# Kernel tuning notes

Measured on AMD Instinct MI355X. Metric: run time of the kernel, lower is better.

Reference implementation:

```python
import jax, jax.numpy as jnp
import numpy as np

N, M = 20000, 5000
D_IN, D_OUT = 256, 512
EPS = 1e-5


def setup_inputs() -> dict:
    key = jax.random.key(0)
    k1, k2, k3, k4 = jax.random.split(key, 4)
    x = jax.random.normal(k1, (N, D_IN), dtype=jnp.float32)
    H = (jax.random.uniform(k2, (N, M)) < 0.05).astype(jnp.float32)
    W_node = jax.random.normal(k3, (D_IN, D_OUT), dtype=jnp.float32) / np.sqrt(D_IN)
    W_res = jax.random.normal(k4, (D_IN, D_OUT), dtype=jnp.float32) / np.sqrt(D_IN)
    gamma = jnp.ones((D_OUT,), dtype=jnp.float32)
    beta = jnp.zeros((D_OUT,), dtype=jnp.float32)
    return {"x": x, "H": H, "W_node": W_node, "W_res": W_res, "gamma": gamma, "beta": beta}


def reference(x, H, W_node, W_res, gamma, beta):
    # degrees, clamped to >= 1
    d_v = jnp.clip(jnp.sum(H, axis=1), 1.0)   # [N] node degree
    d_e = jnp.clip(jnp.sum(H, axis=0), 1.0)   # [M] hyperedge degree
    x_proj = x @ W_node                       # [N, d_out]
    edge_feat = (H.T @ x_proj) / d_e[:, None] # [M, d_out] node -> edge aggregation
    node_update = (H @ edge_feat) / d_v[:, None]  # [N, d_out] edge -> node
    h = node_update + x @ W_res               # residual (d_in != d_out -> linear)
    # LayerNorm over last dim
    mu = jnp.mean(h, axis=-1, keepdims=True)
    var = jnp.mean(jnp.square(h - mu), axis=-1, keepdims=True)
    out = (h - mu) * jax.lax.rsqrt(var + EPS) * gamma + beta
    return out  # dropout is identity at inference
```

## Files before the change

kernel.cpp:

```cpp
#include <hip/hip_runtime.h>


#define N_NODES 20000
#define M_EDGES 5000
#define MPAD    5120
#define NPAD    20480
#define NW      320
#define MW      80
#define DIN     256
#define DOUT    512
#define SPLITS  16
#define SPLITSB 4

typedef short bf16x4 __attribute__((ext_vector_type(4)));
typedef short bf16x8 __attribute__((ext_vector_type(8)));
typedef float f32x4 __attribute__((ext_vector_type(4)));
typedef unsigned long long u64;

#define MFMA16(A, B, C) __builtin_amdgcn_mfma_f32_16x16x32_bf16((A), (B), (C), 0, 0, 0)

__device__ __forceinline__ unsigned short f2b(float f) {
  unsigned u = __builtin_bit_cast(unsigned, f);
  return (unsigned short)((u + 0x7FFFu + ((u >> 16) & 1u)) >> 16);
}

__device__ __forceinline__ void stage16(const void* g, void* l) {
  __builtin_amdgcn_global_load_lds(
      (const __attribute__((address_space(1))) unsigned int*)g,
      (__attribute__((address_space(3))) unsigned int*)l, 16, 0, 0);
}

__device__ __forceinline__ bf16x8 expand8(unsigned b) {
  union { unsigned u[4]; bf16x8 v; } r;
  const unsigned t = b | (b << 15);
  r.u[0] = (t & 0x00010001u) * 0x3F80u;
  r.u[1] = ((t >> 2) & 0x00010001u) * 0x3F80u;
  r.u[2] = ((t >> 4) & 0x00010001u) * 0x3F80u;
  r.u[3] = ((t >> 6) & 0x00010001u) * 0x3F80u;
  return r.v;
}

__global__ __launch_bounds__(256) void prep_kernel(const float* __restrict__ Wn,
                                                   const float* __restrict__ Wr,
                                                   unsigned short* __restrict__ WT) {
  const int q = blockIdx.x * 256 + threadIdx.x;
  const int j = q >> 9, k = q & 511;
  const float v = (k < 256) ? Wn[(size_t)k * 512 + j] : Wr[(size_t)(k - 256) * 512 + j];
  WT[(size_t)j * 512 + k] = f2b(v);
}

__global__ __launch_bounds__(256) void xt_kernel(const float* __restrict__ x,
                                                 unsigned short* __restrict__ xpb) {
  const int j = threadIdx.x;
  const int n8 = blockIdx.x;
  union { unsigned u[4]; bf16x8 v; } o;
#pragma unroll
  for (int p = 0; p < 4; ++p) {
    const int n = n8 * 8 + 2 * p;
    const float v0 = (n < N_NODES) ? x[(size_t)n * DIN + j] : 0.f;
    const float v1 = (n + 1 < N_NODES) ? x[(size_t)(n + 1) * DIN + j] : 0.f;
    o.u[p] = (unsigned)f2b(v0) | ((unsigned)f2b(v1) << 16);
  }
  *(bf16x8*)(xpb + ((size_t)n8 * 256 + j) * 8) = o.v;
}

__global__ __launch_bounds__(256) void pack_kernel(const float* __restrict__ H,
                                                   u64* __restrict__ HTb) {
  const int t = threadIdx.x;
  const int g = blockIdx.x;
  const int h = blockIdx.y;
  const int n0 = g * 64;
  const int mc = h * 1024 + 4 * t;
  u64 h0 = 0, h1 = 0, h2 = 0, h3 = 0;
  if (mc + 3 < M_EDGES) {
    const float* col = H + mc;
#pragma unroll 4
    for (int r = 0; r < 64; ++r) {
      const int n = n0 + r;
      if (n < N_NODES) {
        const float4 v = *(const float4*)(col + (size_t)n * M_EDGES);
        h0 |= (u64)(v.x != 0.f) << r;
        h1 |= (u64)(v.y != 0.f) << r;
        h2 |= (u64)(v.z != 0.f) << r;
        h3 |= (u64)(v.w != 0.f) << r;
      }
    }
  } else if (mc < M_EDGES) {
    for (int r = 0; r < 64; ++r) {
      const int n = n0 + r;
      if (n < N_NODES) {
        const float* row = H + (size_t)n * M_EDGES;
        if (mc + 0 < M_EDGES) h0 |= (u64)(row[mc + 0] != 0.f) << r;
        if (mc + 1 < M_EDGES) h1 |= (u64)(row[mc + 1] != 0.f) << r;
        if (mc + 2 < M_EDGES) h2 |= (u64)(row[mc + 2] != 0.f) << r;
        if (mc + 3 < M_EDGES) h3 |= (u64)(row[mc + 3] != 0.f) << r;
      }
    }
  }
  u64* hp = HTb + (size_t)g * MPAD + mc;
  hp[0] = h0; hp[1] = h1; hp[2] = h2; hp[3] = h3;
}

__global__ __launch_bounds__(256) void bt_kernel(const u64* __restrict__ HTb,
                                                 u64* __restrict__ Hb) {
  const int t = threadIdx.x;
  const int w = t >> 6, l = t & 63;
  const int id = blockIdx.x * 4 + w;
  const int nw = id % NW;
  const int mw = id / NW;
  const u64 word = HTb[(size_t)nw * MPAD + mw * 64 + l];
  u64 out = 0;
  for (int r = 0; r < 64; ++r) {
    const u64 mask = __ballot(((word >> r) & 1ull) != 0);
    if (l == r) out = mask;
  }
  Hb[(size_t)mw * NPAD + nw * 64 + l] = out;
}

__global__ __launch_bounds__(256) void deg_kernel(const u64* __restrict__ Hb,
                                                  const u64* __restrict__ HTb,
                                                  float* __restrict__ inv_de,
                                                  float* __restrict__ inv_dv) {
  const int g = blockIdx.x * 256 + threadIdx.x;
  if (g < MPAD) {
    int c = 0;
    for (int nw = 0; nw < NW; ++nw) c += __popcll(HTb[(size_t)nw * MPAD + g]);
    inv_de[g] = 1.f / fmaxf((float)c, 1.f);
  } else if (g < MPAD + NPAD) {
    const int n = g - MPAD;
    int c = 0;
#pragma unroll
    for (int mw = 0; mw < MW; ++mw) c += __popcll(Hb[(size_t)mw * NPAD + n]);
    inv_dv[n] = 1.f / fmaxf((float)c, 1.f);
  }
}

__global__ __launch_bounds__(256) void gemmA_kernel(const unsigned short* __restrict__ xpb,
                                                    const u64* __restrict__ HTb,
                                                    float* __restrict__ partial) {
  __shared__ char lds[2][16384];
  const int t = threadIdx.x;
  const int w = t >> 6, l = t & 63;
  const int lr = l & 15, lg = l >> 4;
  const int shl8 = lg * 8;
  const int wgid = blockIdx.x;
  const int mchunk = wgid >> 6;
  const int sj = wgid & 63;
  const int s = sj >> 2, jb = sj & 3;
  const int m0 = mchunk * 256 + w * 64;
  const int j0 = jb * 64;

  f32x4 acc[4][4] = {};
  const u64* bbase = HTb + (size_t)(s * 20) * MPAD + m0 + lr;
  const char* xb = (const char*)xpb;
  const int n8b = s * 160;
  const int sj0 = j0 + w * 16 + lr;

  u64 b00, b01, b02, b03, b04, b05, b06, b07;
  u64 b10, b11, b12, b13, b14, b15, b16, b17;

#define GA_LOADB(S, st_) do {                                                  \
    const u64* bp_ = bbase + (size_t)(st_) * 2 * MPAD;                         \
    b##S##0 = bp_[0]; b##S##1 = bp_[16]; b##S##2 = bp_[32]; b##S##3 = bp_[48]; \
    const u64* bq_ = bp_ + MPAD;                                               \
    b##S##4 = bq_[0]; b##S##5 = bq_[16]; b##S##6 = bq_[32]; b##S##7 = bq_[48]; \
  } while (0)

#define GA_STAGE(buf, st_) do {                                                \
    const size_t r0_ = (size_t)(n8b + (st_) * 16 + lg) * 256 + sj0;            \
    stage16(xb + (r0_) * 16,              &lds[buf][(w) * 1024 + l * 16]);     \
    stage16(xb + (r0_ + 4 * 256) * 16,    &lds[buf][(4 + w) * 1024 + l * 16]); \
    stage16(xb + (r0_ + 8 * 256) * 16,    &lds[buf][(8 + w) * 1024 + l * 16]); \
    stage16(xb + (r0_ + 12 * 256) * 16,   &lds[buf][(12 + w) * 1024 + l * 16]);\
  } while (0)

#define GA_JG(jg, BW) do {                                                     \
    const unsigned wlo_ = (unsigned)(BW), whi_ = (unsigned)((BW) >> 32);       \
    const bf16x8 e0_ = expand8((wlo_ >> shl8) & 255u);                         \
    const bf16x8 e1_ = expand8((whi_ >> shl8) & 255u);                         \
    acc[0][jg] = MFMA16(A00_, e0_, acc[0][jg]);                                \
    acc[1][jg] = MFMA16(A10_, e0_, acc[1][jg]);                                \
    acc[2][jg] = MFMA16(A20_, e0_, acc[2][jg]);                                \
    acc[3][jg] = MFMA16(A30_, e0_, acc[3][jg]);                                \
    acc[0][jg] = MFMA16(A01_, e1_, acc[0][jg]);                                \
    acc[1][jg] = MFMA16(A11_, e1_, acc[1][jg]);                                \
    acc[2][jg] = MFMA16(A21_, e1_, acc[2][jg]);                                \
    acc[3][jg] = MFMA16(A31_, e1_, acc[3][jg]);                                \
  } while (0)

#define GA_COMP(buf, h, W0, W1, W2, W3) do {                                   \
    const char* L_ = &lds[buf][(h) * 8192];                                    \
    const bf16x8 A00_ = *(const bf16x8*)(L_ + l * 16 + 0);                     \
    const bf16x8 A10_ = *(const bf16x8*)(L_ + l * 16 + 1024);                  \
    const bf16x8 A20_ = *(const bf16x8*)(L_ + l * 16 + 2048);                  \
    const bf16x8 A30_ = *(const bf16x8*)(L_ + l * 16 + 3072);                  \
    const bf16x8 A01_ = *(const bf16x8*)(L_ + l * 16 + 4096);                  \
    const bf16x8 A11_ = *(const bf16x8*)(L_ + l * 16 + 5120);                  \
    const bf16x8 A21_ = *(const bf16x8*)(L_ + l * 16 + 6144);                  \
    const bf16x8 A31_ = *(const bf16x8*)(L_ + l * 16 + 7168);                  \
    GA_JG(0, W0); GA_JG(1, W1); GA_JG(2, W2); GA_JG(3, W3);                    \
  } while (0)

  GA_LOADB(0, 0);
  GA_STAGE(0, 0);
  for (int st = 0; st < 10; st += 2) {
    const int n1 = (st + 1 < 10) ? st + 1 : 9;
    GA_LOADB(1, n1); GA_STAGE(1, n1);
    asm volatile("s_waitcnt vmcnt(12)" ::: "memory");
    __builtin_amdgcn_s_barrier();
    GA_COMP(0, 0, b00, b01, b02, b03);
    GA_COMP(0, 1, b04, b05, b06, b07);
    __builtin_amdgcn_s_barrier();
    const int n2 = (st + 2 < 10) ? st + 2 : 9;
    GA_LOADB(0, n2); GA_STAGE(0, n2);
    asm volatile("s_waitcnt vmcnt(12)" ::: "memory");
    __builtin_amdgcn_s_barrier();
    GA_COMP(1, 0, b10, b11, b12, b13);
    GA_COMP(1, 1, b14, b15, b16, b17);
    __builtin_amdgcn_s_barrier();
  }
#undef GA_LOADB
#undef GA_STAGE
#undef GA_JG
#undef GA_COMP

  float* pp = partial + (size_t)s * (DIN * MPAD);
#pragma unroll
  for (int fr = 0; fr < 4; ++fr)
#pragma unroll
    for (int r = 0; r < 4; ++r) {
      const int j = j0 + fr * 16 + lg * 4 + r;
#pragma unroll
      for (int jg = 0; jg < 4; ++jg)
        pp[(size_t)j * MPAD + m0 + jg * 16 + lr] = acc[fr][jg][r];
    }
}

__global__ __launch_bounds__(256) void reduceA_kernel(const float* __restrict__ partial,
                                                      const float* __restrict__ inv_de,
                                                      unsigned short* __restrict__ t2p) {
  const int t = threadIdx.x;
  const int m = blockIdx.x * 256 + t;
  const int jc = blockIdx.y * 16;
  const float e = inv_de[m];
  unsigned short* ob = t2p + ((size_t)(m >> 3) * 256) * 8 + (m & 7);
  for (int jj = 0; jj < 16; ++jj) {
    const int j = jc + jj;
    const float* p = partial + (size_t)j * MPAD + m;
    float s = 0.f;
#pragma unroll
    for (int sp = 0; sp < SPLITS; ++sp) s += p[(size_t)sp * (DIN * MPAD)];
    ob[(size_t)j * 8] = f2b(s * e);
  }
}

__global__ __launch_bounds__(256) void gemmB_kernel(const unsigned short* __restrict__ t2p,
                                                    const u64* __restrict__ Hb,
                                                    float* __restrict__ partialB) {
  __shared__ char lds[2][16384];
  const int t = threadIdx.x;
  const int w = t >> 6, l = t & 63;
  const int lr = l & 15, lg = l >> 4;
  const int shl8 = lg * 8;
  const int wgid = blockIdx.x;
  const int nchunk = wgid >> 4;
  const int sj = wgid & 15;
  const int s = sj >> 2, jb = sj & 3;
  const int n0 = nchunk * 256 + w * 64;
  const int j0 = jb * 64;

  f32x4 acc[4][4] = {};
  const u64* abase = Hb + (size_t)(s * 20) * NPAD + n0 + lr;
  const char* tb = (const char*)t2p;
  const int m8b = s * 160;
  const int sj0 = j0 + w * 16 + lr;

  u64 a00, a01, a02, a03, a04, a05, a06, a07;
  u64 a10, a11, a12, a13, a14, a15, a16, a17;

#define GB_LOADA(S, st_) do {                                                  \
    const u64* ap_ = abase + (size_t)(st_) * 2 * NPAD;                         \
    a##S##0 = ap_[0]; a##S##1 = ap_[16]; a##S##2 = ap_[32]; a##S##3 = ap_[48]; \
    const u64* aq_ = ap_ + NPAD;                                               \
    a##S##4 = aq_[0]; a##S##5 = aq_[16]; a##S##6 = aq_[32]; a##S##7 = aq_[48]; \
  } while (0)

#define GB_STAGE(buf, st_) do {                                                \
    const size_t r0_ = (size_t)(m8b + (st_) * 16 + lg) * 256 + sj0;            \
    stage16(tb + (r0_) * 16,              &lds[buf][(w) * 1024 + l * 16]);     \
    stage16(tb + (r0_ + 4 * 256) * 16,    &lds[buf][(4 + w) * 1024 + l * 16]); \
    stage16(tb + (r0_ + 8 * 256) * 16,    &lds[buf][(8 + w) * 1024 + l * 16]); \
    stage16(tb + (r0_ + 12 * 256) * 16,   &lds[buf][(12 + w) * 1024 + l * 16]);\
  } while (0)

#define GB_FR(fr, AW) do {                                                     \
    const unsigned wlo_ = (unsigned)(AW), whi_ = (unsigned)((AW) >> 32);       \
    const bf16x8 e0_ = expand8((wlo_ >> shl8) & 255u);                         \
    const bf16x8 e1_ = expand8((whi_ >> shl8) & 255u);                         \
    acc[fr][0] = MFMA16(e0_, B00_, acc[fr][0]);                                \
    acc[fr][1] = MFMA16(e0_, B10_, acc[fr][1]);                                \
    acc[fr][2] = MFMA16(e0_, B20_, acc[fr][2]);                                \
    acc[fr][3] = MFMA16(e0_, B30_, acc[fr][3]);                                \
    acc[fr][0] = MFMA16(e1_, B01_, acc[fr][0]);                                \
    acc[fr][1] = MFMA16(e1_, B11_, acc[fr][1]);                                \
    acc[fr][2] = MFMA16(e1_, B21_, acc[fr][2]);                                \
    acc[fr][3] = MFMA16(e1_, B31_, acc[fr][3]);                                \
  } while (0)

#define GB_COMP(buf, h, W0, W1, W2, W3) do {                                   \
    const char* L_ = &lds[buf][(h) * 8192];                                    \
    const bf16x8 B00_ = *(const bf16x8*)(L_ + l * 16 + 0);                     \
    const bf16x8 B10_ = *(const bf16x8*)(L_ + l * 16 + 1024);                  \
    const bf16x8 B20_ = *(const bf16x8*)(L_ + l * 16 + 2048);                  \
    const bf16x8 B30_ = *(const bf16x8*)(L_ + l * 16 + 3072);                  \
    const bf16x8 B01_ = *(const bf16x8*)(L_ + l * 16 + 4096);                  \
    const bf16x8 B11_ = *(const bf16x8*)(L_ + l * 16 + 5120);                  \
    const bf16x8 B21_ = *(const bf16x8*)(L_ + l * 16 + 6144);                  \
    const bf16x8 B31_ = *(const bf16x8*)(L_ + l * 16 + 7168);                  \
    GB_FR(0, W0); GB_FR(1, W1); GB_FR(2, W2); GB_FR(3, W3);                    \
  } while (0)

  GB_LOADA(0, 0);
  GB_STAGE(0, 0);
  for (int st = 0; st < 10; st += 2) {
    const int n1 = (st + 1 < 10) ? st + 1 : 9;
    GB_LOADA(1, n1); GB_STAGE(1, n1);
    asm volatile("s_waitcnt vmcnt(12)" ::: "memory");
    __builtin_amdgcn_s_barrier();
    GB_COMP(0, 0, a00, a01, a02, a03);
    GB_COMP(0, 1, a04, a05, a06, a07);
    __builtin_amdgcn_s_barrier();
    const int n2 = (st + 2 < 10) ? st + 2 : 9;
    GB_LOADA(0, n2); GB_STAGE(0, n2);
    asm volatile("s_waitcnt vmcnt(12)" ::: "memory");
    __builtin_amdgcn_s_barrier();
    GB_COMP(1, 0, a10, a11, a12, a13);
    GB_COMP(1, 1, a14, a15, a16, a17);
    __builtin_amdgcn_s_barrier();
  }
#undef GB_LOADA
#undef GB_STAGE
#undef GB_FR
#undef GB_COMP

  float* pp = partialB + (size_t)s * ((size_t)NPAD * DIN);
#pragma unroll
  for (int fr = 0; fr < 4; ++fr) {
#pragma unroll
    for (int r = 0; r < 4; ++r) {
      const int n = n0 + fr * 16 + lg * 4 + r;
#pragma unroll
      for (int jg = 0; jg < 4; ++jg)
        pp[(size_t)n * DIN + j0 + jg * 16 + lr] = acc[fr][jg][r];
    }
  }
}

__global__ __launch_bounds__(256) void reduceB_kernel(const float* __restrict__ partialB,
                                                      const float* __restrict__ inv_dv,
                                                      unsigned short* __restrict__ T3) {
  const size_t idx4 = (size_t)blockIdx.x * 1024 + threadIdx.x * 4;
  f32x4 s = (f32x4){0.f, 0.f, 0.f, 0.f};
#pragma unroll
  for (int sp = 0; sp < SPLITSB; ++sp) {
    const f32x4 a = *(const f32x4*)(partialB + (size_t)sp * ((size_t)NPAD * DIN) + idx4);
#pragma unroll
    for (int i = 0; i < 4; ++i) s[i] += a[i];
  }
  const float dv = inv_dv[idx4 >> 8];
  bf16x4 o;
#pragma unroll
  for (int i = 0; i < 4; ++i) o[i] = (short)f2b(s[i] * dv);
  *(bf16x4*)(T3 + idx4) = o;
}

__global__ __launch_bounds__(512) void gemmC_kernel(const float* __restrict__ x,
                                                    const unsigned short* __restrict__ T3,
                                                    const unsigned short* __restrict__ WT,
                                                    float* __restrict__ out) {
  __shared__ unsigned short As[128 * 64];
  __shared__ unsigned short Bsh[128 * 64];
  const int t = threadIdx.x;
  const int n0 = blockIdx.x * 128;
  const int j0 = blockIdx.y * 128;
  const int w = t >> 6, l = t & 63;
  const int wr = w >> 2, wc = w & 3;
  const int lr = l & 15, lg = l >> 4;
  f32x4 acc[4][2];
#pragma unroll
  for (int i = 0; i < 4; ++i)
#pragma unroll
    for (int jq = 0; jq < 2; ++jq) acc[i][jq] = (f32x4){0.f, 0.f, 0.f, 0.f};
  const int sr = t >> 3, sk8 = t & 7;

  for (int st = 0; st < 8; ++st) {
    __syncthreads();
#pragma unroll
    for (int p = 0; p < 2; ++p) {
      const int node = sr + p * 64;
      const int gn = n0 + node;
      bf16x8 pk;
      if (st < 4) {
        if (gn < N_NODES)
          pk = *(const bf16x8*)(T3 + (size_t)gn * DIN + st * 64 + sk8 * 8);
        else {
#pragma unroll
          for (int jq = 0; jq < 8; ++jq) pk[jq] = 0;
        }
      } else {
        if (gn < N_NODES) {
          const float4* p4 = (const float4*)(x + (size_t)gn * DIN + (st - 4) * 64 + sk8 * 8);
          const float4 q0 = p4[0], q1 = p4[1];
          pk[0] = (short)f2b(q0.x); pk[1] = (short)f2b(q0.y); pk[2] = (short)f2b(q0.z); pk[3] = (short)f2b(q0.w);
          pk[4] = (short)f2b(q1.x); pk[5] = (short)f2b(q1.y); pk[6] = (short)f2b(q1.z); pk[7] = (short)f2b(q1.w);
        } else {
#pragma unroll
          for (int jq = 0; jq < 8; ++jq) pk[jq] = 0;
        }
      }
      *(bf16x8*)((char*)As + node * 128 + ((sk8 * 16) ^ ((node & 7) << 4))) = pk;
    }
#pragma unroll
    for (int p = 0; p < 2; ++p) {
      const int j = sr + p * 64;
      const bf16x8 pk = *(const bf16x8*)(WT + (size_t)(j0 + j) * 512 + st * 64 + sk8 * 8);
      *(bf16x8*)((char*)Bsh + j * 128 + ((sk8 * 16) ^ ((j & 7) << 4))) = pk;
    }
    __syncthreads();
#pragma unroll
    for (int ks = 0; ks < 2; ++ks) {
      const int kb = ks * 64 + 16 * lg;
      bf16x8 bf[2];
#pragma unroll
      for (int fc = 0; fc < 2; ++fc) {
        const int row = wc * 32 + fc * 16 + lr;
        bf[fc] = *(const bf16x8*)((const char*)Bsh + row * 128 + (kb ^ ((row & 7) << 4)));
      }
#pragma unroll
      for (int fr = 0; fr < 4; ++fr) {
        const int row = wr * 64 + fr * 16 + lr;
        const bf16x8 af = *(const bf16x8*)((const char*)As + row * 128 + (kb ^ ((row & 7) << 4)));
#pragma unroll
        for (int fc = 0; fc < 2; ++fc)
          acc[fr][fc] = __builtin_amdgcn_mfma_f32_16x16x32_bf16(af, bf[fc], acc[fr][fc], 0, 0, 0);
      }
    }
  }
#pragma unroll
  for (int fr = 0; fr < 4; ++fr)
#pragma unroll
    for (int fc = 0; fc < 2; ++fc) {
      const int col = j0 + wc * 32 + fc * 16 + lr;
#pragma unroll
      for (int r = 0; r < 4; ++r) {
        const int row = n0 + wr * 64 + fr * 16 + 4 * lg + r;
        if (row < N_NODES) out[(size_t)row * DOUT + col] = acc[fr][fc][r];
      }
    }
}

__global__ __launch_bounds__(256) void ln_kernel(float* __restrict__ out,
                                                 const float* __restrict__ gamma,
                                                 const float* __restrict__ beta) {
  const int row = blockIdx.x * 4 + (threadIdx.x >> 6);
  const int l = threadIdx.x & 63;
  float* p = out + (size_t)row * DOUT;
  float4 va = *(const float4*)(p + 4 * l);
  float4 vb = *(const float4*)(p + 256 + 4 * l);
  float s = va.x + va.y + va.z + va.w + vb.x + vb.y + vb.z + vb.w;
  float s2 = va.x * va.x + va.y * va.y + va.z * va.z + va.w * va.w +
             vb.x * vb.x + vb.y * vb.y + vb.z * vb.z + vb.w * vb.w;
#pragma unroll
  for (int m = 1; m < 64; m <<= 1) { s += __shfl_xor(s, m, 64); s2 += __shfl_xor(s2, m, 64); }
  const float mu = s * (1.f / DOUT);
  const float rs = rsqrtf(s2 * (1.f / DOUT) - mu * mu + 1e-5f);
  const float4 g0 = *(const float4*)(gamma + 4 * l);
  const float4 g1 = *(const float4*)(gamma + 256 + 4 * l);
  const float4 b0 = *(const float4*)(beta + 4 * l);
  const float4 b1 = *(const float4*)(beta + 256 + 4 * l);
  va.x = (va.x - mu) * rs * g0.x + b0.x;  va.y = (va.y - mu) * rs * g0.y + b0.y;
  va.z = (va.z - mu) * rs * g0.z + b0.z;  va.w = (va.w - mu) * rs * g0.w + b0.w;
  vb.x = (vb.x - mu) * rs * g1.x + b1.x;  vb.y = (vb.y - mu) * rs * g1.y + b1.y;
  vb.z = (vb.z - mu) * rs * g1.z + b1.z;  vb.w = (vb.w - mu) * rs * g1.w + b1.w;
  *(float4*)(p + 4 * l) = va;
  *(float4*)(p + 256 + 4 * l) = vb;
}

extern "C" void kernel_launch(void* const* d_in, const int* in_sizes, int n_in,
                              void* d_out, int out_size, void* d_ws, size_t ws_size,
                              hipStream_t stream) {
  (void)in_sizes; (void)n_in; (void)out_size; (void)ws_size;
  const float* x = (const float*)d_in[0];
  const float* H = (const float*)d_in[1];
  const float* Wn = (const float*)d_in[2];
  const float* Wr = (const float*)d_in[3];
  const float* gamma = (const float*)d_in[4];
  const float* beta = (const float*)d_in[5];
  float* out = (float*)d_out;
  char* ws = (char*)d_ws;

  unsigned short* WT  = (unsigned short*)(ws + 0);
  u64* Hb             = (u64*)(ws + 524288);
  u64* HTb            = (u64*)(ws + 13631488);
  float* inv_de       = (float*)(ws + 26738688);
  float* inv_dv       = (float*)(ws + 26759168);
  unsigned short* xpb = (unsigned short*)(ws + 26841088);
  float* partialA     = (float*)(ws + 37326848);
  unsigned short* t2p = (unsigned short*)(ws + 121212928);
  float* partialB     = (float*)(ws + 123834368);
  unsigned short* T3  = (unsigned short*)(ws + 207720448);

  prep_kernel<<<dim3(1024), dim3(256), 0, stream>>>(Wn, Wr, WT);
  xt_kernel<<<dim3(2560), dim3(256), 0, stream>>>(x, xpb);
  pack_kernel<<<dim3(320, 5), dim3(256), 0, stream>>>(H, HTb);
  bt_kernel<<<dim3(6400), dim3(256), 0, stream>>>(HTb, Hb);
  deg_kernel<<<dim3(100), dim3(256), 0, stream>>>(Hb, HTb, inv_de, inv_dv);
  gemmA_kernel<<<dim3(1280), dim3(256), 0, stream>>>(xpb, HTb, partialA);
  reduceA_kernel<<<dim3(20, 16), dim3(256), 0, stream>>>(partialA, inv_de, t2p);
  gemmB_kernel<<<dim3(1280), dim3(256), 0, stream>>>(t2p, Hb, partialB);
  reduceB_kernel<<<dim3(5000), dim3(256), 0, stream>>>(partialB, inv_dv, T3);
  gemmC_kernel<<<dim3(157, 4), dim3(512), 0, stream>>>(x, T3, WT, out);
  ln_kernel<<<dim3(5000), dim3(256), 0, stream>>>(out, gamma, beta);
}
```

Before: 338.6 us.

## Store split-K partials in bf16 and fuse reduceB, final GEMM and LayerNorm

The split-K partial buffers of gemmA and gemmB are now written as bf16 instead of fp32, which halves the traffic of writing and re-reading them in the reduce steps. reduceB, gemmC and ln_kernel are merged into one gemmC2 kernel. Each block owns 64 full rows with all 512 output columns, reduces the partials into LDS, streams a pre-swizzled weight image, and applies LayerNorm in registers before one final write. This removes the T3 round-trip, the extra read and write of out, and two launches. In exchange it adds bf16 rounding error in the partial sums, uses 128KB of LDS per block with low occupancy, and has no overlap between the weight loads and the MFMA work.

```diff
diff --git a/kernel.cpp b/kernel.cpp
--- a/kernel.cpp
+++ b/kernel.cpp
@@ -12,7 +12,6 @@
 #define SPLITS  16
 #define SPLITSB 4
 
-typedef short bf16x4 __attribute__((ext_vector_type(4)));
 typedef short bf16x8 __attribute__((ext_vector_type(8)));
 typedef float f32x4 __attribute__((ext_vector_type(4)));
 typedef unsigned long long u64;
@@ -22,6 +21,10 @@
 __device__ __forceinline__ unsigned short f2b(float f) {
   unsigned u = __builtin_bit_cast(unsigned, f);
   return (unsigned short)((u + 0x7FFFu + ((u >> 16) & 1u)) >> 16);
+}
+
+__device__ __forceinline__ float b2f(unsigned short b) {
+  return __builtin_bit_cast(float, ((unsigned)b) << 16);
 }
 
 __device__ __forceinline__ void stage16(const void* g, void* l) {
@@ -42,11 +45,12 @@
 
 __global__ __launch_bounds__(256) void prep_kernel(const float* __restrict__ Wn,
                                                    const float* __restrict__ Wr,
-                                                   unsigned short* __restrict__ WT) {
+                                                   unsigned short* __restrict__ WTimg) {
   const int q = blockIdx.x * 256 + threadIdx.x;
   const int j = q >> 9, k = q & 511;
   const float v = (k < 256) ? Wn[(size_t)k * 512 + j] : Wr[(size_t)(k - 256) * 512 + j];
-  WT[(size_t)j * 512 + k] = f2b(v);
+  const int byte = (k >> 6) * 65536 + j * 128 + ((((k >> 3) & 7) * 16) ^ ((j & 7) << 4)) + (k & 7) * 2;
+  WTimg[byte >> 1] = f2b(v);
 }
 
 __global__ __launch_bounds__(256) void xt_kernel(const float* __restrict__ x,
@@ -137,7 +141,7 @@
 
 __global__ __launch_bounds__(256) void gemmA_kernel(const unsigned short* __restrict__ xpb,
                                                     const u64* __restrict__ HTb,
-                                                    float* __restrict__ partial) {
+                                                    unsigned short* __restrict__ partial) {
   __shared__ char lds[2][16384];
   const int t = threadIdx.x;
   const int w = t >> 6, l = t & 63;
@@ -224,7 +228,7 @@
 #undef GA_JG
 #undef GA_COMP
 
-  float* pp = partial + (size_t)s * (DIN * MPAD);
+  unsigned short* pp = partial + (size_t)s * (DIN * MPAD);
 #pragma unroll
   for (int fr = 0; fr < 4; ++fr)
 #pragma unroll
@@ -232,11 +236,11 @@
       const int j = j0 + fr * 16 + lg * 4 + r;
 #pragma unroll
       for (int jg = 0; jg < 4; ++jg)
-        pp[(size_t)j * MPAD + m0 + jg * 16 + lr] = acc[fr][jg][r];
-    }
-}
-
-__global__ __launch_bounds__(256) void reduceA_kernel(const float* __restrict__ partial,
+        pp[(size_t)j * MPAD + m0 + jg * 16 + lr] = f2b(acc[fr][jg][r]);
+    }
+}
+
+__global__ __launch_bounds__(256) void reduceA_kernel(const unsigned short* __restrict__ partial,
                                                       const float* __restrict__ inv_de,
                                                       unsigned short* __restrict__ t2p) {
   const int t = threadIdx.x;
@@ -246,17 +250,17 @@
   unsigned short* ob = t2p + ((size_t)(m >> 3) * 256) * 8 + (m & 7);
   for (int jj = 0; jj < 16; ++jj) {
     const int j = jc + jj;
-    const float* p = partial + (size_t)j * MPAD + m;
+    const unsigned short* p = partial + (size_t)j * MPAD + m;
     float s = 0.f;
 #pragma unroll
-    for (int sp = 0; sp < SPLITS; ++sp) s += p[(size_t)sp * (DIN * MPAD)];
+    for (int sp = 0; sp < SPLITS; ++sp) s += b2f(p[(size_t)sp * (DIN * MPAD)]);
     ob[(size_t)j * 8] = f2b(s * e);
   }
 }
 
 __global__ __launch_bounds__(256) void gemmB_kernel(const unsigned short* __restrict__ t2p,
                                                     const u64* __restrict__ Hb,
-                                                    float* __restrict__ partialB) {
+                                                    unsigned short* __restrict__ partialB) {
   __shared__ char lds[2][16384];
   const int t = threadIdx.x;
   const int w = t >> 6, l = t & 63;
@@ -343,7 +347,7 @@
 #undef GB_FR
 #undef GB_COMP
 
-  float* pp = partialB + (size_t)s * ((size_t)NPAD * DIN);
+  unsigned short* pp = partialB + (size_t)s * ((size_t)NPAD * DIN);
 #pragma unroll
   for (int fr = 0; fr < 4; ++fr) {
 #pragma unroll
@@ -351,139 +355,141 @@
       const int n = n0 + fr * 16 + lg * 4 + r;
 #pragma unroll
       for (int jg = 0; jg < 4; ++jg)
-        pp[(size_t)n * DIN + j0 + jg * 16 + lr] = acc[fr][jg][r];
-    }
-  }
-}
-
-__global__ __launch_bounds__(256) void reduceB_kernel(const float* __restrict__ partialB,
-                                                      const float* __restrict__ inv_dv,
-                                                      unsigned short* __restrict__ T3) {
-  const size_t idx4 = (size_t)blockIdx.x * 1024 + threadIdx.x * 4;
-  f32x4 s = (f32x4){0.f, 0.f, 0.f, 0.f};
-#pragma unroll
-  for (int sp = 0; sp < SPLITSB; ++sp) {
-    const f32x4 a = *(const f32x4*)(partialB + (size_t)sp * ((size_t)NPAD * DIN) + idx4);
-#pragma unroll
-    for (int i = 0; i < 4; ++i) s[i] += a[i];
-  }
-  const float dv = inv_dv[idx4 >> 8];
-  bf16x4 o;
-#pragma unroll
-  for (int i = 0; i < 4; ++i) o[i] = (short)f2b(s[i] * dv);
-  *(bf16x4*)(T3 + idx4) = o;
-}
-
-__global__ __launch_bounds__(512) void gemmC_kernel(const float* __restrict__ x,
-                                                    const unsigned short* __restrict__ T3,
-                                                    const unsigned short* __restrict__ WT,
-                                                    float* __restrict__ out) {
-  __shared__ unsigned short As[128 * 64];
-  __shared__ unsigned short Bsh[128 * 64];
+        pp[(size_t)n * DIN + j0 + jg * 16 + lr] = f2b(acc[fr][jg][r]);
+    }
+  }
+}
+
+__global__ __launch_bounds__(512) void gemmC2_kernel(const unsigned short* __restrict__ partialB,
+                                                     const float* __restrict__ inv_dv,
+                                                     const float* __restrict__ x,
+                                                     const unsigned short* __restrict__ WTimg,
+                                                     const float* __restrict__ gamma,
+                                                     const float* __restrict__ beta,
+                                                     float* __restrict__ out) {
+  __shared__ char ldsA[65536];
+  __shared__ char ldsB[65536];
+  __shared__ float lnred[2][64][8];
   const int t = threadIdx.x;
-  const int n0 = blockIdx.x * 128;
-  const int j0 = blockIdx.y * 128;
   const int w = t >> 6, l = t & 63;
-  const int wr = w >> 2, wc = w & 3;
   const int lr = l & 15, lg = l >> 4;
-  f32x4 acc[4][2];
-#pragma unroll
-  for (int i = 0; i < 4; ++i)
-#pragma unroll
-    for (int jq = 0; jq < 2; ++jq) acc[i][jq] = (f32x4){0.f, 0.f, 0.f, 0.f};
-  const int sr = t >> 3, sk8 = t & 7;
-
-  for (int st = 0; st < 8; ++st) {
-    __syncthreads();
-#pragma unroll
-    for (int p = 0; p < 2; ++p) {
-      const int node = sr + p * 64;
-      const int gn = n0 + node;
-      bf16x8 pk;
-      if (st < 4) {
-        if (gn < N_NODES)
-          pk = *(const bf16x8*)(T3 + (size_t)gn * DIN + st * 64 + sk8 * 8);
-        else {
-#pragma unroll
-          for (int jq = 0; jq < 8; ++jq) pk[jq] = 0;
+  const int n0 = blockIdx.x * 64;
+
+  {
+    const int k8 = t & 31;
+    const int rb = t >> 5;
+#pragma unroll
+    for (int pass = 0; pass < 4; ++pass) {
+      const int r = pass * 16 + rb;
+      const size_t base = (size_t)(n0 + r) * 256 + k8 * 8;
+      float sum[8] = {0.f, 0.f, 0.f, 0.f, 0.f, 0.f, 0.f, 0.f};
+#pragma unroll
+      for (int sp = 0; sp < SPLITSB; ++sp) {
+        const bf16x8 v = *(const bf16x8*)(partialB + (size_t)sp * ((size_t)NPAD * DIN) + base);
+#pragma unroll
+        for (int i = 0; i < 8; ++i) sum[i] += b2f((unsigned short)v[i]);
+      }
+      const float dv = inv_dv[n0 + r];
+      union { unsigned u[4]; bf16x8 v; } o;
+#pragma unroll
+      for (int p = 0; p < 4; ++p)
+        o.u[p] = (unsigned)f2b(sum[2 * p] * dv) | ((unsigned)f2b(sum[2 * p + 1] * dv) << 16);
+      *(bf16x8*)(ldsA + r * 1024 + ((k8 * 16) ^ ((r & 7) << 4))) = o.v;
+    }
+  }
+  {
+    const int c4 = t & 63;
+    const int rb = t >> 6;
+#pragma unroll
+    for (int pass = 0; pass < 8; ++pass) {
+      const int r = pass * 8 + rb;
+      float4 v = make_float4(0.f, 0.f, 0.f, 0.f);
+      if (n0 + r < N_NODES) v = *(const float4*)(x + (size_t)(n0 + r) * DIN + c4 * 4);
+      const unsigned u0 = (unsigned)f2b(v.x) | ((unsigned)f2b(v.y) << 16);
+      const unsigned u1 = (unsigned)f2b(v.z) | ((unsigned)f2b(v.w) << 16);
+      const int byte0 = 512 + c4 * 8;
+      const int off = ((byte0 & ~15) ^ ((r & 7) << 4)) + (byte0 & 8);
+      *(uint2*)(ldsA + r * 1024 + off) = make_uint2(u0, u1);
+    }
+  }
+  __syncthreads();
+
+  f32x4 acc[4][4] = {};
+  const int wcol = w * 64;
+  for (int step = 0; step < 8; ++step) {
+    const char* src = (const char*)WTimg + (size_t)step * 65536;
+#pragma unroll
+    for (int i = 0; i < 8; ++i) {
+      const int ofs = (i * 512 + t) * 16;
+      stage16(src + ofs, ldsB + ofs);
+    }
+    asm volatile("s_waitcnt vmcnt(0)" ::: "memory");
+    __builtin_amdgcn_s_barrier();
+#pragma unroll
+    for (int ks = 0; ks < 2; ++ks) {
+      const int kbA = step * 128 + ks * 64 + lg * 16;
+      const int kbB = ks * 64 + lg * 16;
+      bf16x8 bf[4];
+#pragma unroll
+      for (int jg = 0; jg < 4; ++jg) {
+        const int col = wcol + jg * 16 + lr;
+        bf[jg] = *(const bf16x8*)(ldsB + col * 128 + (kbB ^ ((col & 7) << 4)));
+      }
+#pragma unroll
+      for (int fr = 0; fr < 4; ++fr) {
+        const int row = fr * 16 + lr;
+        const bf16x8 af = *(const bf16x8*)(ldsA + row * 1024 + (kbA ^ ((row & 7) << 4)));
+#pragma unroll
+        for (int jg = 0; jg < 4; ++jg)
+          acc[fr][jg] = MFMA16(af, bf[jg], acc[fr][jg]);
+      }
+    }
+    __builtin_amdgcn_s_barrier();
+  }
+
+#pragma unroll
+  for (int fr = 0; fr < 4; ++fr)
+#pragma unroll
+    for (int r = 0; r < 4; ++r) {
+      float s = 0.f, s2 = 0.f;
+#pragma unroll
+      for (int jg = 0; jg < 4; ++jg) {
+        const float v = acc[fr][jg][r];
+        s += v; s2 += v * v;
+      }
+#pragma unroll
+      for (int m = 1; m < 16; m <<= 1) {
+        s += __shfl_xor(s, m, 64);
+        s2 += __shfl_xor(s2, m, 64);
+      }
+      if (lr == 0) {
+        const int row = fr * 16 + lg * 4 + r;
+        lnred[0][row][w] = s;
+        lnred[1][row][w] = s2;
+      }
+    }
+  __syncthreads();
+
+#pragma unroll
+  for (int fr = 0; fr < 4; ++fr) {
+#pragma unroll
+    for (int r = 0; r < 4; ++r) {
+      const int row = fr * 16 + lg * 4 + r;
+      float S = 0.f, S2 = 0.f;
+#pragma unroll
+      for (int ww = 0; ww < 8; ++ww) { S += lnred[0][row][ww]; S2 += lnred[1][row][ww]; }
+      const float mu = S * (1.f / 512.f);
+      const float rs = rsqrtf(S2 * (1.f / 512.f) - mu * mu + 1e-5f);
+      const int gn = n0 + row;
+      if (gn < N_NODES) {
+#pragma unroll
+        for (int jg = 0; jg < 4; ++jg) {
+          const int col = wcol + jg * 16 + lr;
+          out[(size_t)gn * DOUT + col] = (acc[fr][jg][r] - mu) * rs * gamma[col] + beta[col];
         }
-      } else {
-        if (gn < N_NODES) {
-          const float4* p4 = (const float4*)(x + (size_t)gn * DIN + (st - 4) * 64 + sk8 * 8);
-          const float4 q0 = p4[0], q1 = p4[1];
-          pk[0] = (short)f2b(q0.x); pk[1] = (short)f2b(q0.y); pk[2] = (short)f2b(q0.z); pk[3] = (short)f2b(q0.w);
-          pk[4] = (short)f2b(q1.x); pk[5] = (short)f2b(q1.y); pk[6] = (short)f2b(q1.z); pk[7] = (short)f2b(q1.w);
-        } else {
-#pragma unroll
-          for (int jq = 0; jq < 8; ++jq) pk[jq] = 0;
-        }
-      }
-      *(bf16x8*)((char*)As + node * 128 + ((sk8 * 16) ^ ((node & 7) << 4))) = pk;
-    }
-#pragma unroll
-    for (int p = 0; p < 2; ++p) {
-      const int j = sr + p * 64;
-      const bf16x8 pk = *(const bf16x8*)(WT + (size_t)(j0 + j) * 512 + st * 64 + sk8 * 8);
-      *(bf16x8*)((char*)Bsh + j * 128 + ((sk8 * 16) ^ ((j & 7) << 4))) = pk;
-    }
-    __syncthreads();
-#pragma unroll
-    for (int ks = 0; ks < 2; ++ks) {
-      const int kb = ks * 64 + 16 * lg;
-      bf16x8 bf[2];
-#pragma unroll
-      for (int fc = 0; fc < 2; ++fc) {
-        const int row = wc * 32 + fc * 16 + lr;
-        bf[fc] = *(const bf16x8*)((const char*)Bsh + row * 128 + (kb ^ ((row & 7) << 4)));
-      }
-#pragma unroll
-      for (int fr = 0; fr < 4; ++fr) {
-        const int row = wr * 64 + fr * 16 + lr;
-        const bf16x8 af = *(const bf16x8*)((const char*)As + row * 128 + (kb ^ ((row & 7) << 4)));
-#pragma unroll
-        for (int fc = 0; fc < 2; ++fc)
-          acc[fr][fc] = __builtin_amdgcn_mfma_f32_16x16x32_bf16(af, bf[fc], acc[fr][fc], 0, 0, 0);
-      }
-    }
-  }
-#pragma unroll
-  for (int fr = 0; fr < 4; ++fr)
-#pragma unroll
-    for (int fc = 0; fc < 2; ++fc) {
-      const int col = j0 + wc * 32 + fc * 16 + lr;
-#pragma unroll
-      for (int r = 0; r < 4; ++r) {
-        const int row = n0 + wr * 64 + fr * 16 + 4 * lg + r;
-        if (row < N_NODES) out[(size_t)row * DOUT + col] = acc[fr][fc][r];
-      }
-    }
-}
-
-__global__ __launch_bounds__(256) void ln_kernel(float* __restrict__ out,
-                                                 const float* __restrict__ gamma,
-                                                 const float* __restrict__ beta) {
-  const int row = blockIdx.x * 4 + (threadIdx.x >> 6);
-  const int l = threadIdx.x & 63;
-  float* p = out + (size_t)row * DOUT;
-  float4 va = *(const float4*)(p + 4 * l);
-  float4 vb = *(const float4*)(p + 256 + 4 * l);
-  float s = va.x + va.y + va.z + va.w + vb.x + vb.y + vb.z + vb.w;
-  float s2 = va.x * va.x + va.y * va.y + va.z * va.z + va.w * va.w +
-             vb.x * vb.x + vb.y * vb.y + vb.z * vb.z + vb.w * vb.w;
-#pragma unroll
-  for (int m = 1; m < 64; m <<= 1) { s += __shfl_xor(s, m, 64); s2 += __shfl_xor(s2, m, 64); }
-  const float mu = s * (1.f / DOUT);
-  const float rs = rsqrtf(s2 * (1.f / DOUT) - mu * mu + 1e-5f);
-  const float4 g0 = *(const float4*)(gamma + 4 * l);
-  const float4 g1 = *(const float4*)(gamma + 256 + 4 * l);
-  const float4 b0 = *(const float4*)(beta + 4 * l);
-  const float4 b1 = *(const float4*)(beta + 256 + 4 * l);
-  va.x = (va.x - mu) * rs * g0.x + b0.x;  va.y = (va.y - mu) * rs * g0.y + b0.y;
-  va.z = (va.z - mu) * rs * g0.z + b0.z;  va.w = (va.w - mu) * rs * g0.w + b0.w;
-  vb.x = (vb.x - mu) * rs * g1.x + b1.x;  vb.y = (vb.y - mu) * rs * g1.y + b1.y;
-  vb.z = (vb.z - mu) * rs * g1.z + b1.z;  vb.w = (vb.w - mu) * rs * g1.w + b1.w;
-  *(float4*)(p + 4 * l) = va;
-  *(float4*)(p + 256 + 4 * l) = vb;
+      }
+    }
+  }
 }
 
 extern "C" void kernel_launch(void* const* d_in, const int* in_sizes, int n_in,
@@ -499,18 +505,17 @@
   float* out = (float*)d_out;
   char* ws = (char*)d_ws;
 
-  unsigned short* WT  = (unsigned short*)(ws + 0);
-  u64* Hb             = (u64*)(ws + 524288);
-  u64* HTb            = (u64*)(ws + 13631488);
-  float* inv_de       = (float*)(ws + 26738688);
-  float* inv_dv       = (float*)(ws + 26759168);
-  unsigned short* xpb = (unsigned short*)(ws + 26841088);
-  float* partialA     = (float*)(ws + 37326848);
-  unsigned short* t2p = (unsigned short*)(ws + 121212928);
-  float* partialB     = (float*)(ws + 123834368);
-  unsigned short* T3  = (unsigned short*)(ws + 207720448);
-
-  prep_kernel<<<dim3(1024), dim3(256), 0, stream>>>(Wn, Wr, WT);
+  unsigned short* WTimg    = (unsigned short*)(ws + 0);
+  u64* Hb                  = (u64*)(ws + 524288);
+  u64* HTb                 = (u64*)(ws + 13631488);
+  float* inv_de            = (float*)(ws + 26738688);
+  float* inv_dv            = (float*)(ws + 26759168);
+  unsigned short* xpb      = (unsigned short*)(ws + 26841088);
+  unsigned short* partialA = (unsigned short*)(ws + 37326848);
+  unsigned short* t2p      = (unsigned short*)(ws + 79269888);
+  unsigned short* partialB = (unsigned short*)(ws + 81891328);
+
+  prep_kernel<<<dim3(1024), dim3(256), 0, stream>>>(Wn, Wr, WTimg);
   xt_kernel<<<dim3(2560), dim3(256), 0, stream>>>(x, xpb);
   pack_kernel<<<dim3(320, 5), dim3(256), 0, stream>>>(H, HTb);
   bt_kernel<<<dim3(6400), dim3(256), 0, stream>>>(HTb, Hb);
@@ -518,7 +523,6 @@
   gemmA_kernel<<<dim3(1280), dim3(256), 0, stream>>>(xpb, HTb, partialA);
   reduceA_kernel<<<dim3(20, 16), dim3(256), 0, stream>>>(partialA, inv_de, t2p);
   gemmB_kernel<<<dim3(1280), dim3(256), 0, stream>>>(t2p, Hb, partialB);
-  reduceB_kernel<<<dim3(5000), dim3(256), 0, stream>>>(partialB, inv_dv, T3);
-  gemmC_kernel<<<dim3(157, 4), dim3(512), 0, stream>>>(x, T3, WT, out);
-  ln_kernel<<<dim3(5000), dim3(256), 0, stream>>>(out, gamma, beta);
-}
+  gemmC2_kernel<<<dim3(313), dim3(512), 0, stream>>>(partialB, inv_dv, x, WTimg,
+                                                     gamma, beta, out);
+}
```

After: 341.0 us. Within noise of the previous version (+0.7%).
